# Optimization experiments

Hardware: AMD Instinct MI355X
Metric: run time of the kernel (lower is better)

The kernel has to match this reference:

```python
import jax, jax.numpy as jnp
import numpy as np

B, T, C, H = 4096, 32, 180, 6
HD = C // H  # 30
EPS = 1e-5

def _ln(x, g, b):
    mu = jnp.mean(x, axis=-1, keepdims=True)
    var = jnp.mean(jnp.square(x - mu), axis=-1, keepdims=True)
    return (x - mu) * jax.lax.rsqrt(var + EPS) * g + b

def setup_inputs() -> dict:
    key = jax.random.key(0)
    ks = jax.random.split(key, 12)
    s_in = 1.0 / np.sqrt(C)
    s_ff = 1.0 / np.sqrt(4 * C)
    return {
        "x": jax.random.normal(ks[0], (B, T, C), jnp.float32),
        "wq": jax.random.normal(ks[1], (H, C, HD), jnp.float32) * s_in,
        "wk": jax.random.normal(ks[2], (H, C, HD), jnp.float32) * s_in,
        "wv": jax.random.normal(ks[3], (H, C, HD), jnp.float32) * s_in,
        "g1": jnp.ones((C,), jnp.float32),
        "be1": jnp.zeros((C,), jnp.float32),
        "g2": jnp.ones((C,), jnp.float32),
        "be2": jnp.zeros((C,), jnp.float32),
        "w1": jax.random.normal(ks[4], (C, 4 * C), jnp.float32) * s_in,
        "b1": jnp.zeros((4 * C,), jnp.float32),
        "w2": jax.random.normal(ks[5], (4 * C, C), jnp.float32) * s_ff,
        "b2": jnp.zeros((C,), jnp.float32),
    }

def reference(x, wq, wk, wv, g1, be1, g2, be2, w1, b1, w2, b2):
    Bv, Tv, Cv = x.shape
    h = _ln(x, g1, be1)
    # batched multi-head QKV (replaces per-head Python loop)
    q = jnp.einsum('btc,hcd->bhtd', h, wq)
    k = jnp.einsum('btc,hcd->bhtd', h, wk)
    v = jnp.einsum('btc,hcd->bhtd', h, wv)
    scores = jnp.einsum('bhtd,bhsd->bhts', q, k) * (HD ** -0.5)
    mask = jnp.tril(jnp.ones((Tv, Tv), bool))
    scores = jnp.where(mask, scores, -jnp.inf)
    attn = jax.nn.softmax(scores, axis=-1)  # dropout off (eval)
    out = jnp.einsum('bhts,bhsd->bhtd', attn, v)
    out = jnp.transpose(out, (0, 2, 1, 3)).reshape(Bv, Tv, Cv)  # concat heads
    x = x + out
    h2 = _ln(x, g2, be2)
    mlp = jax.nn.relu(h2 @ w1 + b1) @ w2 + b2  # dropout off (eval)
    return x + mlp
```

## Files before the change

kernel.cpp:

```cpp
#include <hip/hip_runtime.h>

typedef __attribute__((ext_vector_type(8))) short short8;
typedef __attribute__((ext_vector_type(4))) float f32x4;
typedef unsigned short ushort_t;
typedef unsigned int u32;
typedef unsigned long long u64;

#define MFMA16(a,b,c) __builtin_amdgcn_mfma_f32_16x16x32_bf16((a),(b),(c),0,0,0)

__device__ __forceinline__ ushort_t f2bf(float f){
  union { float f; u32 u; } v; v.f = f;
  u32 r = v.u + 0x7fffu + ((v.u >> 16) & 1u);
  return (ushort_t)(r >> 16);
}
__device__ __forceinline__ float bf2f(ushort_t h){
  union { u32 u; float f; } v; v.u = ((u32)h) << 16; return v.f;
}
__device__ __forceinline__ u64 pack4(float a, float b, float c, float d){
  u32 p0 = (u32)f2bf(a) | ((u32)f2bf(b) << 16);
  u32 p1 = (u32)f2bf(c) | ((u32)f2bf(d) << 16);
  return (u64)p0 | ((u64)p1 << 32);
}
__device__ __forceinline__ void pin(short8 &v){ asm volatile("" : "+v"(v)); }

template<int CTRL>
__device__ __forceinline__ float dpp_add(float x){
  union { float f; int i; } a, b;
  a.f = x;
  b.i = __builtin_amdgcn_update_dpp(a.i, a.i, CTRL, 0xF, 0xF, false);
  return x + b.f;
}
__device__ __forceinline__ float red4_add(float x){
  x = dpp_add<0xB1>(x); x = dpp_add<0x4E>(x);
  return x;
}

#define WQKV_ELEMS (576*192)
#define W1T_ELEMS  (768*192)
#define W2T_ELEMS  (192*768)

#define SH 200
#define SS 40

__global__ void prep_weights(const float* __restrict__ wq, const float* __restrict__ wk,
                             const float* __restrict__ wv, const float* __restrict__ w1,
                             const float* __restrict__ w2, ushort_t* __restrict__ ws){
  ushort_t* wqkv = ws;
  ushort_t* w1t = ws + WQKV_ELEMS;
  ushort_t* w2t = w1t + W1T_ELEMS;
  int tid = blockIdx.x * blockDim.x + threadIdx.x;
  int stride = gridDim.x * blockDim.x;
  for (int i = tid; i < WQKV_ELEMS; i += stride){
    int k = i % 192; int row = i / 192;
    int d = row & 31; int m = (row >> 5) % 3; int h = row / 96;
    float v = 0.f;
    if (d < 30 && k < 180){
      const float* W = (m == 0) ? wq : ((m == 1) ? wk : wv);
      v = W[(h*180 + k)*30 + d];
    }
    wqkv[i] = f2bf(v);
  }
  for (int i = tid; i < W1T_ELEMS; i += stride){
    int c = i % 192; int n = i / 192;
    float v = (n < 720 && c < 180) ? w1[c*720 + n] : 0.f;
    w1t[i] = f2bf(v);
  }
  for (int i = tid; i < W2T_ELEMS; i += stride){
    int c4 = i % 768; int n = i / 768;
    float v = (n < 180 && c4 < 720) ? w2[c4*180 + n] : 0.f;
    w2t[i] = f2bf(v);
  }
}

__global__ __launch_bounds__(256, 2)
void block_kernel(const float* __restrict__ x,
                  const float* __restrict__ g1, const float* __restrict__ be1,
                  const float* __restrict__ g2, const float* __restrict__ be2,
                  const float* __restrict__ b1, const float* __restrict__ b2,
                  const ushort_t* __restrict__ wqkv, const ushort_t* __restrict__ w1t,
                  const ushort_t* __restrict__ w2t, float* __restrict__ out){
  __shared__ __align__(16) ushort_t W[64*SH];
  __shared__ __align__(16) ushort_t hn[64*SH];
  __shared__ __align__(16) ushort_t att[64*SH];

  int tid = threadIdx.x;
  int wave = tid >> 6, lane = tid & 63;
  int quad = lane >> 4, c16 = lane & 15;
  long base = (long)blockIdx.x * 11520;

  {
    int row = tid >> 2, sub = tid & 3;
    int c0 = sub*48;
    f32x4 xv[12];
    float s1 = 0.f, s2 = 0.f;
    #pragma unroll
    for (int gi = 0; gi < 12; gi++){
      int c = c0 + gi*4;
      if (c < 180) xv[gi] = *(const f32x4*)(x + base + (long)row*180 + c);
      else         xv[gi] = (f32x4)0.f;
      s1 += xv[gi].x + xv[gi].y + xv[gi].z + xv[gi].w;
      s2 += xv[gi].x*xv[gi].x + xv[gi].y*xv[gi].y + xv[gi].z*xv[gi].z + xv[gi].w*xv[gi].w;
    }
    s1 = red4_add(s1); s2 = red4_add(s2);
    float mu = s1 * (1.f/180.f);
    float rstd = rsqrtf(s2 * (1.f/180.f) - mu*mu + 1e-5f);
    #pragma unroll
    for (int gi = 0; gi < 12; gi++){
      int c = c0 + gi*4;
      if (c < 180){
        f32x4 gg = *(const f32x4*)(g1 + c);
        f32x4 bb = *(const f32x4*)(be1 + c);
        *(u64*)(hn + row*SH + c) = pack4((xv[gi].x - mu)*rstd*gg.x + bb.x,
                                         (xv[gi].y - mu)*rstd*gg.y + bb.y,
                                         (xv[gi].z - mu)*rstd*gg.z + bb.z,
                                         (xv[gi].w - mu)*rstd*gg.w + bb.w);
      } else {
        *(u64*)(hn + row*SH + c) = 0ull;
      }
    }
  }
  __syncthreads();

  {
    ushort_t* buf0 = W + wave*(2*32*SS);
    ushort_t* buf1 = buf0 + 32*SS;
    const float scl = 0.18257418583505537f;

    for (int jj = 0; jj < 3; jj++){
      int j = wave*3 + jj;
      int bb = (j >= 6) ? 1 : 0;
      int head = j - 6*bb;
      const ushort_t* wbase = wqkv + head*(96*192);

      f32x4 accq[2][2], acck[2][2], accv[2][2];
      #pragma unroll
      for (int i = 0; i < 2; i++)
        #pragma unroll
        for (int jx = 0; jx < 2; jx++){ accq[i][jx]=(f32x4)0.f; acck[i][jx]=(f32x4)0.f; accv[i][jx]=(f32x4)0.f; }

      short8 aqw[2][6], akw[2][6];
      #pragma unroll
      for (int mt = 0; mt < 2; mt++)
        #pragma unroll
        for (int kk = 0; kk < 6; kk++){
          aqw[mt][kk] = *(const short8*)(wbase + (      mt*16 + c16)*192 + kk*32 + quad*8);
          akw[mt][kk] = *(const short8*)(wbase + (32  + mt*16 + c16)*192 + kk*32 + quad*8);
          pin(aqw[mt][kk]); pin(akw[mt][kk]);
        }
      short8 avc[2], avn[2];
      #pragma unroll
      for (int mt = 0; mt < 2; mt++)
        avc[mt] = *(const short8*)(wbase + (64 + mt*16 + c16)*192 + quad*8);
      #pragma unroll
      for (int kk = 0; kk < 6; kk++){
        if (kk < 5){
          #pragma unroll
          for (int mt = 0; mt < 2; mt++)
            avn[mt] = *(const short8*)(wbase + (64 + mt*16 + c16)*192 + (kk+1)*32 + quad*8);
        }
        short8 hf[2];
        #pragma unroll
        for (int nt = 0; nt < 2; nt++)
          hf[nt] = *(const short8*)(hn + (bb*32 + nt*16 + c16)*SH + kk*32 + quad*8);
        #pragma unroll
        for (int mt = 0; mt < 2; mt++)
          #pragma unroll
          for (int nt = 0; nt < 2; nt++){
            accq[mt][nt] = MFMA16(aqw[mt][kk], hf[nt], accq[mt][nt]);
            acck[mt][nt] = MFMA16(akw[mt][kk], hf[nt], acck[mt][nt]);
            accv[mt][nt] = MFMA16(hf[mt], avc[nt], accv[mt][nt]);
          }
        if (kk < 5){
          #pragma unroll
          for (int mt = 0; mt < 2; mt++) avc[mt] = avn[mt];
        }
      }
      #pragma unroll
      for (int mt = 0; mt < 2; mt++)
        #pragma unroll
        for (int nt = 0; nt < 2; nt++){
          *(u64*)(buf0 + (nt*16 + c16)*SS + mt*16 + quad*4) =
            pack4(accq[mt][nt][0], accq[mt][nt][1], accq[mt][nt][2], accq[mt][nt][3]);
          *(u64*)(buf1 + (nt*16 + c16)*SS + mt*16 + quad*4) =
            pack4(acck[mt][nt][0], acck[mt][nt][1], acck[mt][nt][2], acck[mt][nt][3]);
        }
      f32x4 sacc[2][2];
      #pragma unroll
      for (int i = 0; i < 2; i++){ sacc[i][0]=(f32x4)0.f; sacc[i][1]=(f32x4)0.f; }
      short8 akf[2], bqf[2];
      #pragma unroll
      for (int mt = 0; mt < 2; mt++) akf[mt] = *(const short8*)(buf1 + (mt*16 + c16)*SS + quad*8);
      #pragma unroll
      for (int nt = 0; nt < 2; nt++) bqf[nt] = *(const short8*)(buf0 + (nt*16 + c16)*SS + quad*8);
      #pragma unroll
      for (int mt = 0; mt < 2; mt++)
        #pragma unroll
        for (int nt = 0; nt < 2; nt++)
          sacc[mt][nt] = MFMA16(akf[mt], bqf[nt], sacc[mt][nt]);
      #pragma unroll
      for (int nt = 0; nt < 2; nt++){
        int t = nt*16 + c16;
        float v[8];
        #pragma unroll
        for (int r = 0; r < 4; r++){
          int s0 = quad*4 + r, s1v = 16 + quad*4 + r;
          v[r]   = (s0  > t) ? -1e30f : sacc[0][nt][r]*scl;
          v[4+r] = (s1v > t) ? -1e30f : sacc[1][nt][r]*scl;
        }
        float m = v[0];
        #pragma unroll
        for (int i = 1; i < 8; i++) m = fmaxf(m, v[i]);
        m = fmaxf(m, __shfl_xor(m, 16));
        m = fmaxf(m, __shfl_xor(m, 32));
        float e[8], s = 0.f;
        #pragma unroll
        for (int i = 0; i < 8; i++){ e[i] = __expf(v[i] - m); s += e[i]; }
        s += __shfl_xor(s, 16);
        s += __shfl_xor(s, 32);
        float inv = 1.f / s;
        *(u64*)(buf1 + t*SS +      quad*4) = pack4(e[0]*inv, e[1]*inv, e[2]*inv, e[3]*inv);
        *(u64*)(buf1 + t*SS + 16 + quad*4) = pack4(e[4]*inv, e[5]*inv, e[6]*inv, e[7]*inv);
      }
      #pragma unroll
      for (int mt = 0; mt < 2; mt++)
        #pragma unroll
        for (int nt = 0; nt < 2; nt++)
          *(u64*)(buf0 + (nt*16 + c16)*SS + mt*16 + quad*4) =
            pack4(accv[mt][nt][0], accv[mt][nt][1], accv[mt][nt][2], accv[mt][nt][3]);
      f32x4 oacc[2][2];
      #pragma unroll
      for (int i = 0; i < 2; i++){ oacc[i][0]=(f32x4)0.f; oacc[i][1]=(f32x4)0.f; }
      short8 avf[2], bpf[2];
      #pragma unroll
      for (int mt = 0; mt < 2; mt++) avf[mt] = *(const short8*)(buf0 + (mt*16 + c16)*SS + quad*8);
      #pragma unroll
      for (int nt = 0; nt < 2; nt++) bpf[nt] = *(const short8*)(buf1 + (nt*16 + c16)*SS + quad*8);
      #pragma unroll
      for (int mt = 0; mt < 2; mt++)
        #pragma unroll
        for (int nt = 0; nt < 2; nt++){
          oacc[mt][nt] = MFMA16(avf[mt], bpf[nt], oacc[mt][nt]);
          *(u64*)(att + (bb*32 + nt*16 + c16)*SH + head*32 + mt*16 + quad*4) =
            pack4(oacc[mt][nt][0], oacc[mt][nt][1], oacc[mt][nt][2], oacc[mt][nt][3]);
        }
    }
  }
  __syncthreads();

  #pragma unroll
  for (int it = 0; it < 12; it++){
    int idx = it*256 + tid;
    if (idx < 2880){
      f32x4 v = *(const f32x4*)(x + base + (long)idx*4);
      int row = (int)(((u32)idx * 745655u) >> 25);
      int col4 = (idx - row*45)*4;
      #pragma unroll
      for (int e = 0; e < 4; e++){
        int c = col4 + e;
        int h = (c*4370) >> 17;
        int d = c - h*30;
        v[e] += bf2f(att[row*SH + h*32 + d]);
      }
      *(f32x4*)(out + base + (long)idx*4) = v;
      *(u64*)(hn + row*SH + col4) = pack4(v.x, v.y, v.z, v.w);
    } else {
      int p = idx - 2880;
      int row = (p*21846) >> 16;
      int g = p - row*3;
      *(u64*)(hn + row*SH + 180 + g*4) = 0ull;
    }
  }
  __syncthreads();

  {
    int row = tid >> 2, sub = tid & 3;
    int c0 = sub*48;
    float s1 = 0.f, s2 = 0.f;
    u64 mv[12];
    #pragma unroll
    for (int gi = 0; gi < 12; gi++){
      mv[gi] = *(const u64*)(hn + row*SH + c0 + gi*4);
      #pragma unroll
      for (int e = 0; e < 4; e++){
        float v = bf2f((ushort_t)(mv[gi] >> (16*e)));
        s1 += v; s2 += v*v;
      }
    }
    s1 = red4_add(s1); s2 = red4_add(s2);
    float mu = s1 * (1.f/180.f);
    float rstd = rsqrtf(s2 * (1.f/180.f) - mu*mu + 1e-5f);
    #pragma unroll
    for (int gi = 0; gi < 12; gi++){
      int c = c0 + gi*4;
      if (c < 180){
        f32x4 gg = *(const f32x4*)(g2 + c);
        f32x4 bb = *(const f32x4*)(be2 + c);
        float v0 = (bf2f((ushort_t)(mv[gi]    )) - mu)*rstd*gg.x + bb.x;
        float v1 = (bf2f((ushort_t)(mv[gi]>>16)) - mu)*rstd*gg.y + bb.y;
        float v2 = (bf2f((ushort_t)(mv[gi]>>32)) - mu)*rstd*gg.z + bb.z;
        float v3 = (bf2f((ushort_t)(mv[gi]>>48)) - mu)*rstd*gg.w + bb.w;
        *(u64*)(hn + row*SH + c) = pack4(v0, v1, v2, v3);
      }
    }
  }
  __syncthreads();

  {
    ushort_t* act = W;
    f32x4 outacc[4][3];
    #pragma unroll
    for (int i = 0; i < 4; i++)
      #pragma unroll
      for (int jx = 0; jx < 3; jx++) outacc[i][jx] = (f32x4)0.f;

    for (int ch = 0; ch < 4; ch++){
      f32x4 aacc[3][4];
      #pragma unroll
      for (int i = 0; i < 3; i++)
        #pragma unroll
        for (int jx = 0; jx < 4; jx++) aacc[i][jx] = (f32x4)0.f;
      short8 aw[3][6];
      #pragma unroll
      for (int mi = 0; mi < 3; mi++)
        #pragma unroll
        for (int kk = 0; kk < 6; kk++){
          aw[mi][kk] = *(const short8*)(w1t + (size_t)(ch*192 + (wave*3+mi)*16 + c16)*192 + kk*32 + quad*8);
          pin(aw[mi][kk]);
        }
      #pragma unroll
      for (int kk = 0; kk < 6; kk++){
        short8 bh[4];
        #pragma unroll
        for (int tt = 0; tt < 4; tt++)
          bh[tt] = *(const short8*)(hn + (tt*16 + c16)*SH + kk*32 + quad*8);
        #pragma unroll
        for (int mi = 0; mi < 3; mi++)
          #pragma unroll
          for (int tt = 0; tt < 4; tt++)
            aacc[mi][tt] = MFMA16(aw[mi][kk], bh[tt], aacc[mi][tt]);
      }
      __syncthreads();
      #pragma unroll
      for (int mi = 0; mi < 3; mi++){
        int nrel = (wave*3+mi)*16 + quad*4;
        int nabs = ch*192 + nrel;
        f32x4 bias = (f32x4)0.f;
        if (nabs < 720) bias = *(const f32x4*)(b1 + nabs);
        #pragma unroll
        for (int tt = 0; tt < 4; tt++){
          float v0 = fmaxf(aacc[mi][tt][0] + bias[0], 0.f);
          float v1 = fmaxf(aacc[mi][tt][1] + bias[1], 0.f);
          float v2 = fmaxf(aacc[mi][tt][2] + bias[2], 0.f);
          float v3 = fmaxf(aacc[mi][tt][3] + bias[3], 0.f);
          *(u64*)(act + (tt*16 + c16)*SH + nrel) = pack4(v0, v1, v2, v3);
        }
      }
      __syncthreads();
      short8 bw[3][6];
      #pragma unroll
      for (int ntl = 0; ntl < 3; ntl++)
        #pragma unroll
        for (int kk = 0; kk < 6; kk++){
          bw[ntl][kk] = *(const short8*)(w2t + (size_t)(wave*48 + ntl*16 + c16)*768 + ch*192 + kk*32 + quad*8);
          pin(bw[ntl][kk]);
        }
      #pragma unroll
      for (int kk = 0; kk < 6; kk++){
        short8 aa[4];
        #pragma unroll
        for (int tt = 0; tt < 4; tt++)
          aa[tt] = *(const short8*)(act + (tt*16 + c16)*SH + kk*32 + quad*8);
        #pragma unroll
        for (int tt = 0; tt < 4; tt++)
          #pragma unroll
          for (int ntl = 0; ntl < 3; ntl++)
            outacc[tt][ntl] = MFMA16(aa[tt], bw[ntl][kk], outacc[tt][ntl]);
      }
    }
    #pragma unroll
    for (int ntl = 0; ntl < 3; ntl++){
      int no = wave*48 + ntl*16 + c16;
      if (no < 180){
        float bias = b2[no];
        #pragma unroll
        for (int tt = 0; tt < 4; tt++){
          #pragma unroll
          for (int r = 0; r < 4; r++){
            long a = base + (long)(tt*16 + quad*4 + r)*180 + no;
            out[a] = out[a] + outacc[tt][ntl][r] + bias;
          }
        }
      }
    }
  }
}

extern "C" void kernel_launch(void* const* d_in, const int* in_sizes, int n_in,
                              void* d_out, int out_size, void* d_ws, size_t ws_size,
                              hipStream_t stream) {
  const float* x   = (const float*)d_in[0];
  const float* wq  = (const float*)d_in[1];
  const float* wk  = (const float*)d_in[2];
  const float* wv  = (const float*)d_in[3];
  const float* g1  = (const float*)d_in[4];
  const float* be1 = (const float*)d_in[5];
  const float* g2  = (const float*)d_in[6];
  const float* be2 = (const float*)d_in[7];
  const float* w1  = (const float*)d_in[8];
  const float* b1  = (const float*)d_in[9];
  const float* w2  = (const float*)d_in[10];
  const float* b2  = (const float*)d_in[11];
  ushort_t* ws   = (ushort_t*)d_ws;
  ushort_t* wqkv = ws;
  ushort_t* w1t  = ws + WQKV_ELEMS;
  ushort_t* w2t  = w1t + W1T_ELEMS;
  float* out = (float*)d_out;

  prep_weights<<<512, 256, 0, stream>>>(wq, wk, wv, w1, w2, ws);
  block_kernel<<<2048, 256, 0, stream>>>(x, g1, be1, g2, be2, b1, b2,
                                         wqkv, w1t, w2t, out);
}
```

Baseline: 503.3 us.

## Process one sequence per block to cut LDS and raise occupancy

Each block now handles one 32-token sequence instead of two. This halves the shared-memory buffers, doubles the grid, and raises the launch-bounds occupancy target from 2 to 3 blocks per CU. The attention loop is reorganised to give one head per wave, with the V projection computed after the softmax to lower register pressure. Attention output is stored in a compact 180-column layout so the residual add reads it with a single vectorised load. In exchange, every block reloads the MLP and QKV weight fragments, so weight reuse per block is halved and MLP MFMA tiles get smaller.

```diff
diff --git a/kernel.cpp b/kernel.cpp
--- a/kernel.cpp
+++ b/kernel.cpp
@@ -20,6 +20,9 @@
   u32 p0 = (u32)f2bf(a) | ((u32)f2bf(b) << 16);
   u32 p1 = (u32)f2bf(c) | ((u32)f2bf(d) << 16);
   return (u64)p0 | ((u64)p1 << 32);
+}
+__device__ __forceinline__ u32 pack2(float a, float b){
+  return (u32)f2bf(a) | ((u32)f2bf(b) << 16);
 }
 __device__ __forceinline__ void pin(short8 &v){ asm volatile("" : "+v"(v)); }
 
@@ -41,6 +44,7 @@
 
 #define SH 200
 #define SS 40
+#define SA 184
 
 __global__ void prep_weights(const float* __restrict__ wq, const float* __restrict__ wk,
                              const float* __restrict__ wv, const float* __restrict__ w1,
@@ -72,40 +76,41 @@
   }
 }
 
-__global__ __launch_bounds__(256, 2)
+__global__ __launch_bounds__(256, 3)
 void block_kernel(const float* __restrict__ x,
                   const float* __restrict__ g1, const float* __restrict__ be1,
                   const float* __restrict__ g2, const float* __restrict__ be2,
                   const float* __restrict__ b1, const float* __restrict__ b2,
                   const ushort_t* __restrict__ wqkv, const ushort_t* __restrict__ w1t,
                   const ushort_t* __restrict__ w2t, float* __restrict__ out){
-  __shared__ __align__(16) ushort_t W[64*SH];
-  __shared__ __align__(16) ushort_t hn[64*SH];
-  __shared__ __align__(16) ushort_t att[64*SH];
+  __shared__ __align__(16) ushort_t W[4*2*32*SS];
+  __shared__ __align__(16) ushort_t hn[32*SH];
+  __shared__ __align__(16) ushort_t att[32*SA];
 
   int tid = threadIdx.x;
   int wave = tid >> 6, lane = tid & 63;
   int quad = lane >> 4, c16 = lane & 15;
-  long base = (long)blockIdx.x * 11520;
+  long base = (long)blockIdx.x * 5760;
 
   {
-    int row = tid >> 2, sub = tid & 3;
-    int c0 = sub*48;
-    f32x4 xv[12];
+    int row = tid >> 3, sub = tid & 7;
+    int c0 = sub*24;
+    f32x4 xv[6];
     float s1 = 0.f, s2 = 0.f;
     #pragma unroll
-    for (int gi = 0; gi < 12; gi++){
+    for (int gi = 0; gi < 6; gi++){
       int c = c0 + gi*4;
       if (c < 180) xv[gi] = *(const f32x4*)(x + base + (long)row*180 + c);
       else         xv[gi] = (f32x4)0.f;
       s1 += xv[gi].x + xv[gi].y + xv[gi].z + xv[gi].w;
       s2 += xv[gi].x*xv[gi].x + xv[gi].y*xv[gi].y + xv[gi].z*xv[gi].z + xv[gi].w*xv[gi].w;
     }
-    s1 = red4_add(s1); s2 = red4_add(s2);
+    s1 = red4_add(s1); s1 += __shfl_xor(s1, 4);
+    s2 = red4_add(s2); s2 += __shfl_xor(s2, 4);
     float mu = s1 * (1.f/180.f);
     float rstd = rsqrtf(s2 * (1.f/180.f) - mu*mu + 1e-5f);
     #pragma unroll
-    for (int gi = 0; gi < 12; gi++){
+    for (int gi = 0; gi < 6; gi++){
       int c = c0 + gi*4;
       if (c < 180){
         f32x4 gg = *(const f32x4*)(g1 + c);
@@ -126,18 +131,16 @@
     ushort_t* buf1 = buf0 + 32*SS;
     const float scl = 0.18257418583505537f;
 
-    for (int jj = 0; jj < 3; jj++){
-      int j = wave*3 + jj;
-      int bb = (j >= 6) ? 1 : 0;
-      int head = j - 6*bb;
+    for (int jj = 0; jj < 2; jj++){
+      int head = wave + jj*4;
+      if (head >= 6) break;
       const ushort_t* wbase = wqkv + head*(96*192);
 
-      f32x4 accq[2][2], acck[2][2], accv[2][2];
+      f32x4 accq[2][2], acck[2][2];
       #pragma unroll
       for (int i = 0; i < 2; i++)
         #pragma unroll
-        for (int jx = 0; jx < 2; jx++){ accq[i][jx]=(f32x4)0.f; acck[i][jx]=(f32x4)0.f; accv[i][jx]=(f32x4)0.f; }
-
+        for (int jx = 0; jx < 2; jx++){ accq[i][jx]=(f32x4)0.f; acck[i][jx]=(f32x4)0.f; }
       short8 aqw[2][6], akw[2][6];
       #pragma unroll
       for (int mt = 0; mt < 2; mt++)
@@ -147,33 +150,19 @@
           akw[mt][kk] = *(const short8*)(wbase + (32  + mt*16 + c16)*192 + kk*32 + quad*8);
           pin(aqw[mt][kk]); pin(akw[mt][kk]);
         }
-      short8 avc[2], avn[2];
-      #pragma unroll
-      for (int mt = 0; mt < 2; mt++)
-        avc[mt] = *(const short8*)(wbase + (64 + mt*16 + c16)*192 + quad*8);
       #pragma unroll
       for (int kk = 0; kk < 6; kk++){
-        if (kk < 5){
-          #pragma unroll
-          for (int mt = 0; mt < 2; mt++)
-            avn[mt] = *(const short8*)(wbase + (64 + mt*16 + c16)*192 + (kk+1)*32 + quad*8);
-        }
         short8 hf[2];
         #pragma unroll
         for (int nt = 0; nt < 2; nt++)
-          hf[nt] = *(const short8*)(hn + (bb*32 + nt*16 + c16)*SH + kk*32 + quad*8);
+          hf[nt] = *(const short8*)(hn + (nt*16 + c16)*SH + kk*32 + quad*8);
         #pragma unroll
         for (int mt = 0; mt < 2; mt++)
           #pragma unroll
           for (int nt = 0; nt < 2; nt++){
             accq[mt][nt] = MFMA16(aqw[mt][kk], hf[nt], accq[mt][nt]);
             acck[mt][nt] = MFMA16(akw[mt][kk], hf[nt], acck[mt][nt]);
-            accv[mt][nt] = MFMA16(hf[mt], avc[nt], accv[mt][nt]);
           }
-        if (kk < 5){
-          #pragma unroll
-          for (int mt = 0; mt < 2; mt++) avc[mt] = avn[mt];
-        }
       }
       #pragma unroll
       for (int mt = 0; mt < 2; mt++)
@@ -221,6 +210,29 @@
         *(u64*)(buf1 + t*SS +      quad*4) = pack4(e[0]*inv, e[1]*inv, e[2]*inv, e[3]*inv);
         *(u64*)(buf1 + t*SS + 16 + quad*4) = pack4(e[4]*inv, e[5]*inv, e[6]*inv, e[7]*inv);
       }
+      f32x4 accv[2][2];
+      #pragma unroll
+      for (int i = 0; i < 2; i++){ accv[i][0]=(f32x4)0.f; accv[i][1]=(f32x4)0.f; }
+      short8 avw[2][6];
+      #pragma unroll
+      for (int nt = 0; nt < 2; nt++)
+        #pragma unroll
+        for (int kk = 0; kk < 6; kk++){
+          avw[nt][kk] = *(const short8*)(wbase + (64 + nt*16 + c16)*192 + kk*32 + quad*8);
+          pin(avw[nt][kk]);
+        }
+      #pragma unroll
+      for (int kk = 0; kk < 6; kk++){
+        short8 hf[2];
+        #pragma unroll
+        for (int mt = 0; mt < 2; mt++)
+          hf[mt] = *(const short8*)(hn + (mt*16 + c16)*SH + kk*32 + quad*8);
+        #pragma unroll
+        for (int mt = 0; mt < 2; mt++)
+          #pragma unroll
+          for (int nt = 0; nt < 2; nt++)
+            accv[mt][nt] = MFMA16(hf[mt], avw[nt][kk], accv[mt][nt]);
+      }
       #pragma unroll
       for (int mt = 0; mt < 2; mt++)
         #pragma unroll
@@ -238,33 +250,42 @@
       #pragma unroll
       for (int mt = 0; mt < 2; mt++)
         #pragma unroll
+        for (int nt = 0; nt < 2; nt++)
+          oacc[mt][nt] = MFMA16(avf[mt], bpf[nt], oacc[mt][nt]);
+      #pragma unroll
+      for (int mt = 0; mt < 2; mt++)
+        #pragma unroll
         for (int nt = 0; nt < 2; nt++){
-          oacc[mt][nt] = MFMA16(avf[mt], bpf[nt], oacc[mt][nt]);
-          *(u64*)(att + (bb*32 + nt*16 + c16)*SH + head*32 + mt*16 + quad*4) =
-            pack4(oacc[mt][nt][0], oacc[mt][nt][1], oacc[mt][nt][2], oacc[mt][nt][3]);
+          int t = nt*16 + c16;
+          int c = head*30 + mt*16 + quad*4;
+          ushort_t* p = att + t*SA + c;
+          if (mt == 0 || quad < 3){
+            *(u32*)(p    ) = pack2(oacc[mt][nt][0], oacc[mt][nt][1]);
+            *(u32*)(p + 2) = pack2(oacc[mt][nt][2], oacc[mt][nt][3]);
+          } else {
+            *(u32*)(p    ) = pack2(oacc[mt][nt][0], oacc[mt][nt][1]);
+          }
         }
     }
   }
   __syncthreads();
 
   #pragma unroll
-  for (int it = 0; it < 12; it++){
+  for (int it = 0; it < 6; it++){
     int idx = it*256 + tid;
-    if (idx < 2880){
+    if (idx < 1440){
       f32x4 v = *(const f32x4*)(x + base + (long)idx*4);
       int row = (int)(((u32)idx * 745655u) >> 25);
       int col4 = (idx - row*45)*4;
-      #pragma unroll
-      for (int e = 0; e < 4; e++){
-        int c = col4 + e;
-        int h = (c*4370) >> 17;
-        int d = c - h*30;
-        v[e] += bf2f(att[row*SH + h*32 + d]);
-      }
+      u64 m = *(const u64*)(att + row*SA + col4);
+      v.x += bf2f((ushort_t)(m      ));
+      v.y += bf2f((ushort_t)(m >> 16));
+      v.z += bf2f((ushort_t)(m >> 32));
+      v.w += bf2f((ushort_t)(m >> 48));
       *(f32x4*)(out + base + (long)idx*4) = v;
       *(u64*)(hn + row*SH + col4) = pack4(v.x, v.y, v.z, v.w);
     } else {
-      int p = idx - 2880;
+      int p = idx - 1440;
       int row = (p*21846) >> 16;
       int g = p - row*3;
       *(u64*)(hn + row*SH + 180 + g*4) = 0ull;
@@ -273,12 +294,12 @@
   __syncthreads();
 
   {
-    int row = tid >> 2, sub = tid & 3;
-    int c0 = sub*48;
+    int row = tid >> 3, sub = tid & 7;
+    int c0 = sub*24;
     float s1 = 0.f, s2 = 0.f;
-    u64 mv[12];
-    #pragma unroll
-    for (int gi = 0; gi < 12; gi++){
+    u64 mv[6];
+    #pragma unroll
+    for (int gi = 0; gi < 6; gi++){
       mv[gi] = *(const u64*)(hn + row*SH + c0 + gi*4);
       #pragma unroll
       for (int e = 0; e < 4; e++){
@@ -286,11 +307,12 @@
         s1 += v; s2 += v*v;
       }
     }
-    s1 = red4_add(s1); s2 = red4_add(s2);
+    s1 = red4_add(s1); s1 += __shfl_xor(s1, 4);
+    s2 = red4_add(s2); s2 += __shfl_xor(s2, 4);
     float mu = s1 * (1.f/180.f);
     float rstd = rsqrtf(s2 * (1.f/180.f) - mu*mu + 1e-5f);
     #pragma unroll
-    for (int gi = 0; gi < 12; gi++){
+    for (int gi = 0; gi < 6; gi++){
       int c = c0 + gi*4;
       if (c < 180){
         f32x4 gg = *(const f32x4*)(g2 + c);
@@ -307,18 +329,18 @@
 
   {
     ushort_t* act = W;
-    f32x4 outacc[4][3];
-    #pragma unroll
-    for (int i = 0; i < 4; i++)
+    f32x4 outacc[2][3];
+    #pragma unroll
+    for (int i = 0; i < 2; i++)
       #pragma unroll
       for (int jx = 0; jx < 3; jx++) outacc[i][jx] = (f32x4)0.f;
 
     for (int ch = 0; ch < 4; ch++){
-      f32x4 aacc[3][4];
+      f32x4 aacc[3][2];
       #pragma unroll
       for (int i = 0; i < 3; i++)
         #pragma unroll
-        for (int jx = 0; jx < 4; jx++) aacc[i][jx] = (f32x4)0.f;
+        for (int jx = 0; jx < 2; jx++) aacc[i][jx] = (f32x4)0.f;
       short8 aw[3][6];
       #pragma unroll
       for (int mi = 0; mi < 3; mi++)
@@ -329,14 +351,14 @@
         }
       #pragma unroll
       for (int kk = 0; kk < 6; kk++){
-        short8 bh[4];
-        #pragma unroll
-        for (int tt = 0; tt < 4; tt++)
+        short8 bh[2];
+        #pragma unroll
+        for (int tt = 0; tt < 2; tt++)
           bh[tt] = *(const short8*)(hn + (tt*16 + c16)*SH + kk*32 + quad*8);
         #pragma unroll
         for (int mi = 0; mi < 3; mi++)
           #pragma unroll
-          for (int tt = 0; tt < 4; tt++)
+          for (int tt = 0; tt < 2; tt++)
             aacc[mi][tt] = MFMA16(aw[mi][kk], bh[tt], aacc[mi][tt]);
       }
       __syncthreads();
@@ -347,7 +369,7 @@
         f32x4 bias = (f32x4)0.f;
         if (nabs < 720) bias = *(const f32x4*)(b1 + nabs);
         #pragma unroll
-        for (int tt = 0; tt < 4; tt++){
+        for (int tt = 0; tt < 2; tt++){
           float v0 = fmaxf(aacc[mi][tt][0] + bias[0], 0.f);
           float v1 = fmaxf(aacc[mi][tt][1] + bias[1], 0.f);
           float v2 = fmaxf(aacc[mi][tt][2] + bias[2], 0.f);
@@ -366,12 +388,12 @@
         }
       #pragma unroll
       for (int kk = 0; kk < 6; kk++){
-        short8 aa[4];
-        #pragma unroll
-        for (int tt = 0; tt < 4; tt++)
+        short8 aa[2];
+        #pragma unroll
+        for (int tt = 0; tt < 2; tt++)
           aa[tt] = *(const short8*)(act + (tt*16 + c16)*SH + kk*32 + quad*8);
         #pragma unroll
-        for (int tt = 0; tt < 4; tt++)
+        for (int tt = 0; tt < 2; tt++)
           #pragma unroll
           for (int ntl = 0; ntl < 3; ntl++)
             outacc[tt][ntl] = MFMA16(aa[tt], bw[ntl][kk], outacc[tt][ntl]);
@@ -383,7 +405,7 @@
       if (no < 180){
         float bias = b2[no];
         #pragma unroll
-        for (int tt = 0; tt < 4; tt++){
+        for (int tt = 0; tt < 2; tt++){
           #pragma unroll
           for (int r = 0; r < 4; r++){
             long a = base + (long)(tt*16 + quad*4 + r)*180 + no;
@@ -417,6 +439,6 @@
   float* out = (float*)d_out;
 
   prep_weights<<<512, 256, 0, stream>>>(wq, wk, wv, w1, w2, ws);
-  block_kernel<<<2048, 256, 0, stream>>>(x, g1, be1, g2, be2, b1, b2,
+  block_kernel<<<4096, 256, 0, stream>>>(x, g1, be1, g2, be2, b1, b2,
                                          wqkv, w1t, w2t, out);
 }
```

Measured after the change: 589.0 us. 1.17x slower.
